# Performance work log

Hardware: AMD Instinct MI355X
Metric: run time of the kernel (lower is better)

Reference implementation:

```python
import jax, jax.numpy as jnp
import numpy as np

WIDTH = 64
HEIGHT = 64
FEAT = 128
LAT = 64
NUM_SLOTS = 7


def pixel_coords(img_size):
    g = jnp.linspace(-1.0, 1.0, img_size)
    g1, g2 = jnp.meshgrid(g, g, indexing='ij')  # matches torch.meshgrid default
    return jnp.stack([g1, g2], axis=0)[None]  # (1, 2, S, S)


def clamp_pg(x, lo, hi):
    # clamp that preserves gradients (straight-through)
    return x + jax.lax.stop_gradient(jnp.clip(x, lo, hi) - x)


def setup_inputs() -> dict:
    key = jax.random.key(0)
    k0, k1, k2, k3 = jax.random.split(key, 4)
    bs = 64
    x = jax.random.normal(k0, (bs, FEAT, WIDTH, HEIGHT), jnp.float32)
    rand_pixel = jax.random.uniform(k1, (bs, 1, WIDTH, HEIGHT), jnp.float32)
    conv_w = jax.random.normal(k2, (LAT, FEAT), jnp.float32) / np.sqrt(FEAT)
    conv_b = jax.random.normal(k3, (LAT,), jnp.float32) * 0.01
    gate = jnp.asarray(0.5, jnp.float32)  # ScalarGate parameter (nonzero so c_f is non-degenerate)
    # laplacian kernel: sigma_init = 1 / (sqrt(num_slots) * log 2)
    log_sigma = jnp.asarray(np.log(1.0 / (np.sqrt(NUM_SLOTS) * np.log(2.0))), jnp.float32)
    return {'x': x, 'rand_pixel': rand_pixel, 'conv_w': conv_w, 'conv_b': conv_b,
            'gate': gate, 'log_sigma': log_sigma, 'num_cl_steps': 6}


def _forward(x, rand_pixel, conv_w, conv_b, gate, log_sigma, num_cl_steps):
    bs = x.shape[0]
    # SemiConv: gated 1x1 conv + fixed uv coordinate channels
    out = gate * (jnp.einsum('of,bfhw->bohw', conv_w, x) + conv_b[None, :, None, None])
    uv = jnp.concatenate([jnp.zeros((1, LAT - 2, WIDTH, HEIGHT), out.dtype),
                          pixel_coords(WIDTH).astype(out.dtype)], axis=1)
    c_f = out + uv                      # (bs, LAT, W, H)
    delta = out[:, -2:]                 # (bs, 2, W, H)
    sigma = jnp.exp(log_sigma)
    c_flat = c_f.reshape(bs, LAT, -1)   # (bs, LAT, W*H)
    b_idx = jnp.arange(bs)
    log_s0 = jnp.zeros((bs, 1, WIDTH, HEIGHT), c_f.dtype)

    def step(log_s, _):
        # interpolate-to-same-size is identity -> scope = exp(log_s)
        probs = (rand_pixel * jnp.exp(log_s)).reshape(bs, -1)
        idx = jnp.argmax(probs, axis=1)                 # (bs,)
        seed = c_flat[b_idx, :, idx]                    # (bs, LAT)
        diff = c_f - seed[:, :, None, None]
        dist = jnp.sqrt(clamp_pg((diff ** 2).sum(1), 1e-10, 1e10))  # euclidian (laplacian kernel)
        alpha = jnp.exp(-dist / sigma)[:, None]         # (bs, 1, W, H)
        alpha = clamp_pg(alpha, 0.01, 0.99)
        log_m = log_s + jnp.log(alpha)
        new_log_s = log_s + jnp.log1p(-alpha)
        return new_log_s, (log_m, new_log_s, seed)

    log_s_final, (log_m_steps, log_s_steps, seeds) = jax.lax.scan(
        step, log_s0, None, length=num_cl_steps)
    # log_m_k has num_cl_steps masks plus the final scope appended
    log_m_k = jnp.concatenate([log_m_steps, log_s_final[None]], axis=0)
    log_s_k = jnp.concatenate([log_s0[None], log_s_steps], axis=0)
    return log_m_k, log_s_k, c_f, delta, seeds


def reference(x, rand_pixel, conv_w, conv_b, gate, log_sigma, num_cl_steps):
    return _forward(x, rand_pixel, conv_w, conv_b, gate, log_sigma, num_cl_steps)
```

## Files before the change

kernel.cpp:

```cpp
#include <hip/hip_runtime.h>
#include <hip/hip_bf16.h>

#define NPIX 4096
#define FEAT 128
#define LAT 64
#define BS 64
#define NSTEPS 6

#define OFF_LOGM  0u
#define OFF_LOGS  1835008u
#define OFF_CF    3670016u
#define OFF_DELTA 20447232u
#define OFF_SEEDS 20971520u

typedef float f32x4 __attribute__((ext_vector_type(4)));
typedef short s16x8 __attribute__((ext_vector_type(8)));

__device__ __forceinline__ void amax_comb(float& bv, int& bi, float v, int i) {
    if (v > bv || (v == bv && i < bi)) { bv = v; bi = i; }
}

__device__ __forceinline__ short f2bf_rne(float r) {
    __hip_bfloat16 h = __float2bfloat16(r);
    return __builtin_bit_cast(short, h);
}

__device__ __forceinline__ void split2(float v, short& hi, short& lo) {
    unsigned u = __builtin_bit_cast(unsigned, v);
    hi = (short)(u >> 16);
    float hf = __builtin_bit_cast(float, u & 0xFFFF0000u);
    lo = f2bf_rne(v - hf);
}

__device__ __forceinline__ void transpose4(float4& v, int b) {
    float4 w;
    w.x = __shfl_xor(v.x, 1, 64); w.y = __shfl_xor(v.y, 1, 64);
    w.z = __shfl_xor(v.z, 1, 64); w.w = __shfl_xor(v.w, 1, 64);
    float4 u;
    if ((b & 1) == 0) u = make_float4(v.x, w.x, v.z, w.z);
    else              u = make_float4(w.y, v.y, w.w, v.w);
    float4 w2;
    w2.x = __shfl_xor(u.x, 2, 64); w2.y = __shfl_xor(u.y, 2, 64);
    w2.z = __shfl_xor(u.z, 2, 64); w2.w = __shfl_xor(u.w, 2, 64);
    if ((b & 2) == 0) v = make_float4(u.x, u.y, w2.x, w2.y);
    else              v = make_float4(w2.z, w2.w, u.z, u.w);
}

__global__ void prep_w(const float* __restrict__ w, const float* __restrict__ gate_p,
                       short* __restrict__ gwh, short* __restrict__ gwl)
{
    int i = blockIdx.x * 256 + threadIdx.x;
    float v = gate_p[0] * w[i];
    short h, l; split2(v, h, l);
    gwh[i] = h; gwl[i] = l;
}

__global__ __launch_bounds__(512, 4) void conv_mfma(
    const float* __restrict__ x, const float* __restrict__ rand_pixel,
    const float* __restrict__ bias, const float* __restrict__ gate_p,
    float* __restrict__ out,
    float* __restrict__ pval, int* __restrict__ pidx, int* __restrict__ cnt,
    const short* __restrict__ gwh, const short* __restrict__ gwl)
{
    __shared__ __align__(16) short Xhi[256][40];
    __shared__ __align__(16) short Xlo[256][40];
    __shared__ __align__(16) short Whi[64][132];
    __shared__ __align__(16) short Wlo[64][132];
    __shared__ float sbias[64];

    const int tid  = threadIdx.x;
    const int b    = blockIdx.x >> 4;
    const int tile = blockIdx.x & 15;
    const int p0   = tile * 256;
    const int lane = tid & 63;
    const int wv   = tid >> 6;
    const int l15  = lane & 15;
    const int lg   = lane >> 4;
    const int oh   = wv >> 2;
    const int pxq  = wv & 3;

    const int q  = tid >> 2;
    const int j  = tid & 3;
    const int P  = (q & 63) * 4;
    const int g0 = q >> 6;

    if (tile == 0 && tid < 8) cnt[b * 8 + tid] = 0;
    if (tid < 64) sbias[tid] = gate_p[0] * bias[tid];

    {
        const int o = tid >> 3, c = (tid & 7) * 16;
        *(s16x8*)&Whi[o][c]     = *(const s16x8*)&gwh[o * 128 + c];
        *(s16x8*)&Whi[o][c + 8] = *(const s16x8*)&gwh[o * 128 + c + 8];
        *(s16x8*)&Wlo[o][c]     = *(const s16x8*)&gwl[o * 128 + c];
        *(s16x8*)&Wlo[o][c + 8] = *(const s16x8*)&gwl[o * 128 + c + 8];
    }

    const float* xb = x + (size_t)b * FEAT * NPIX + p0;
    float4 v[4];
    #pragma unroll
    for (int i = 0; i < 4; ++i) {
        int g = g0 + 2 * i;
        v[i] = *(const float4*)(xb + (size_t)(g * 4 + j) * NPIX + P);
    }
    #pragma unroll
    for (int i = 0; i < 4; ++i) {
        int g = g0 + 2 * i;
        float4 t = v[i]; transpose4(t, j);
        short h0, l0, h1, l1, h2, l2, h3, l3;
        split2(t.x, h0, l0); split2(t.y, h1, l1);
        split2(t.z, h2, l2); split2(t.w, h3, l3);
        *(short4*)&Xhi[P + j][g * 4] = make_short4(h0, h1, h2, h3);
        *(short4*)&Xlo[P + j][g * 4] = make_short4(l0, l1, l2, l3);
    }
    __syncthreads();

    f32x4 acc[2][4];
    #pragma unroll
    for (int og2 = 0; og2 < 2; ++og2)
        #pragma unroll
        for (int pg = 0; pg < 4; ++pg)
            acc[og2][pg] = (f32x4){0.f, 0.f, 0.f, 0.f};

    #pragma unroll
    for (int kc = 0; kc < 4; ++kc) {
        if (kc < 3) {
            #pragma unroll
            for (int i = 0; i < 4; ++i) {
                int g = g0 + 2 * i;
                v[i] = *(const float4*)(xb + (size_t)((kc + 1) * 32 + g * 4 + j) * NPIX + P);
            }
        }

        s16x8 Ah[2], Al[2];
        #pragma unroll
        for (int og2 = 0; og2 < 2; ++og2) {
            int o = oh * 32 + og2 * 16 + l15;
            Ah[og2] = *(const s16x8*)&Whi[o][kc * 32 + lg * 8];
            Al[og2] = *(const s16x8*)&Wlo[o][kc * 32 + lg * 8];
        }

        #pragma unroll
        for (int pg = 0; pg < 4; ++pg) {
            int pxl = pxq * 64 + pg * 16 + l15;
            s16x8 Bh = *(const s16x8*)&Xhi[pxl][lg * 8];
            s16x8 Bl = *(const s16x8*)&Xlo[pxl][lg * 8];
            #pragma unroll
            for (int og2 = 0; og2 < 2; ++og2) {
                acc[og2][pg] = __builtin_amdgcn_mfma_f32_16x16x32_bf16(Ah[og2], Bh, acc[og2][pg], 0, 0, 0);
                acc[og2][pg] = __builtin_amdgcn_mfma_f32_16x16x32_bf16(Ah[og2], Bl, acc[og2][pg], 0, 0, 0);
                acc[og2][pg] = __builtin_amdgcn_mfma_f32_16x16x32_bf16(Al[og2], Bh, acc[og2][pg], 0, 0, 0);
            }
        }

        if (kc < 3) {
            __syncthreads();
            #pragma unroll
            for (int i = 0; i < 4; ++i) {
                int g = g0 + 2 * i;
                float4 t = v[i]; transpose4(t, j);
                short h0, l0, h1, l1, h2, l2, h3, l3;
                split2(t.x, h0, l0); split2(t.y, h1, l1);
                split2(t.z, h2, l2); split2(t.w, h3, l3);
                *(short4*)&Xhi[P + j][g * 4] = make_short4(h0, h1, h2, h3);
                *(short4*)&Xlo[P + j][g * 4] = make_short4(l0, l1, l2, l3);
            }
            __syncthreads();
        }
    }

    float* cf = out + OFF_CF + (size_t)b * LAT * NPIX;
    #pragma unroll
    for (int og2 = 0; og2 < 2; ++og2) {
        #pragma unroll
        for (int pg = 0; pg < 4; ++pg) {
            #pragma unroll
            for (int r = 0; r < 4; ++r) {
                int o = oh * 32 + og2 * 16 + lg * 4 + r;
                int p = p0 + pxq * 64 + pg * 16 + l15;
                float vv = acc[og2][pg][r] + sbias[o];
                if (o == 62) {
                    out[OFF_DELTA + ((size_t)b * 2 + 0) * NPIX + p] = vv;
                    vv += (float)(-1.0 + 2.0 * (double)(p >> 6) / 63.0);
                } else if (o == 63) {
                    out[OFF_DELTA + ((size_t)b * 2 + 1) * NPIX + p] = vv;
                    vv += (float)(-1.0 + 2.0 * (double)(p & 63) / 63.0);
                }
                cf[(size_t)o * NPIX + p] = vv;
            }
        }
    }

    if (wv == 0) {
        *(float4*)(out + OFF_LOGS + (size_t)b * NPIX + p0 + lane * 4) =
            make_float4(0.f, 0.f, 0.f, 0.f);
        float4 rv = *(const float4*)(rand_pixel + (size_t)b * NPIX + p0 + lane * 4);
        int pb = p0 + lane * 4;
        float bv = rv.x; int bi = pb;
        if (rv.y > bv) { bv = rv.y; bi = pb + 1; }
        if (rv.z > bv) { bv = rv.z; bi = pb + 2; }
        if (rv.w > bv) { bv = rv.w; bi = pb + 3; }
        #pragma unroll
        for (int off = 32; off > 0; off >>= 1) {
            float ov = __shfl_down(bv, off, 64);
            int   oi = __shfl_down(bi, off, 64);
            amax_comb(bv, bi, ov, oi);
        }
        if (lane == 0) { pval[blockIdx.x] = bv; pidx[blockIdx.x] = bi; }
    }
}

#define REP16(OP) OP(0) OP(1) OP(2) OP(3) OP(4) OP(5) OP(6) OP(7) \
                  OP(8) OP(9) OP(10) OP(11) OP(12) OP(13) OP(14) OP(15)

__global__ __launch_bounds__(1024) void steps_fused(
    const float* __restrict__ rand_pixel, const float* __restrict__ log_sigma_p,
    float* __restrict__ out, float* pv, int* pi, int* cnt)
{
    __shared__ float s_mv[16];
    __shared__ int   s_mi[16];
    __shared__ __align__(16) float s_seed[LAT];
    __shared__ float s_rv[16];
    __shared__ int   s_ri[16];

    const int tid  = threadIdx.x;
    const int b    = blockIdx.x >> 2;
    const int tile = blockIdx.x & 3;
    const int p    = tile * 1024 + tid;

    const float* cfb = out + OFF_CF + (size_t)b * LAT * NPIX;

#define DECLR(i) f32x4 r##i;
    REP16(DECLR)
#define LOADR(i) r##i = (f32x4){ cfb[(size_t)(4*i+0)*NPIX + p], cfb[(size_t)(4*i+1)*NPIX + p], \
                                 cfb[(size_t)(4*i+2)*NPIX + p], cfb[(size_t)(4*i+3)*NPIX + p] };
    REP16(LOADR)

    f32x4 aq = r0 * r0;
#define SQR(i) aq += r##i * r##i;
    SQR(1) SQR(2) SQR(3) SQR(4) SQR(5) SQR(6) SQR(7)
    SQR(8) SQR(9) SQR(10) SQR(11) SQR(12) SQR(13) SQR(14) SQR(15)
    const float cr2 = aq[0] + aq[1] + aq[2] + aq[3];

    const float rp    = rand_pixel[(size_t)b * NPIX + p];
    const float sigma = expf(log_sigma_p[0]);
    float ls = 0.f;

    #pragma unroll 1
    for (int s = 0; s < NSTEPS; ++s) {
        if (s > 0) {
            if (tid == 0) {
                while (__hip_atomic_load(&cnt[b * 8 + s], __ATOMIC_ACQUIRE,
                                         __HIP_MEMORY_SCOPE_AGENT) < 4)
                    __builtin_amdgcn_s_sleep(2);
            }
            __syncthreads();
        }
        const int nmerge = (s == 0) ? 16 : 4;
        if (tid < nmerge) {
            s_mv[tid] = __hip_atomic_load(&pv[(s * BS + b) * 16 + tid],
                                          __ATOMIC_RELAXED, __HIP_MEMORY_SCOPE_AGENT);
            s_mi[tid] = __hip_atomic_load(&pi[(s * BS + b) * 16 + tid],
                                          __ATOMIC_RELAXED, __HIP_MEMORY_SCOPE_AGENT);
        }
        __syncthreads();

        float bv = -1.0f; int bi = 0;
        for (int k = 0; k < nmerge; ++k) amax_comb(bv, bi, s_mv[k], s_mi[k]);

        if (tid < LAT) s_seed[tid] = cfb[(size_t)tid * NPIX + bi];
        __syncthreads();
        if (tile == 0 && tid < LAT)
            out[OFF_SEEDS + ((size_t)s * BS + b) * LAT + tid] = s_seed[tid];

        f32x4 dacc = (f32x4){0.f, 0.f, 0.f, 0.f};
        f32x4 sacc = (f32x4){0.f, 0.f, 0.f, 0.f};
#define DOT(i) { f32x4 sv = *(const f32x4*)&s_seed[4*i]; dacc += r##i * sv; sacc += sv * sv; }
        REP16(DOT)
        float dot = dacc[0] + dacc[1] + dacc[2] + dacc[3];
        float s2  = sacc[0] + sacc[1] + sacc[2] + sacc[3];
        float d2  = cr2 + s2 - 2.0f * dot;

        float dist  = sqrtf(fminf(fmaxf(d2, 1e-10f), 1e10f));
        float alpha = expf(-dist / sigma);
        alpha = fminf(fmaxf(alpha, 0.01f), 0.99f);
        float lm  = ls + logf(alpha);
        float lsn = ls + log1pf(-alpha);

        out[OFF_LOGM + ((size_t)s * BS + b) * NPIX + p]       = lm;
        out[OFF_LOGS + ((size_t)(s + 1) * BS + b) * NPIX + p] = lsn;
        ls = lsn;

        if (s == NSTEPS - 1) {
            out[OFF_LOGM + ((size_t)NSTEPS * BS + b) * NPIX + p] = lsn;
        } else {
            float prob = rp * expf(lsn);
            int   idx  = p;
            #pragma unroll
            for (int off = 32; off > 0; off >>= 1) {
                float ov = __shfl_down(prob, off, 64);
                int   oi = __shfl_down(idx, off, 64);
                amax_comb(prob, idx, ov, oi);
            }
            int lane = tid & 63, wid = tid >> 6;
            if (lane == 0) { s_rv[wid] = prob; s_ri[wid] = idx; }
            __syncthreads();
            if (tid == 0) {
                float fb = s_rv[0]; int fi = s_ri[0];
                #pragma unroll
                for (int k = 1; k < 16; ++k) amax_comb(fb, fi, s_rv[k], s_ri[k]);
                __hip_atomic_store(&pv[((s + 1) * BS + b) * 16 + tile], fb,
                                   __ATOMIC_RELAXED, __HIP_MEMORY_SCOPE_AGENT);
                __hip_atomic_store(&pi[((s + 1) * BS + b) * 16 + tile], fi,
                                   __ATOMIC_RELAXED, __HIP_MEMORY_SCOPE_AGENT);
                __hip_atomic_fetch_add(&cnt[b * 8 + s + 1], 1,
                                       __ATOMIC_RELEASE, __HIP_MEMORY_SCOPE_AGENT);
            }
        }
    }
}

__global__ __launch_bounds__(1024) void step_kernel(
    const float* __restrict__ rand_pixel, const float* __restrict__ log_sigma_p,
    float* __restrict__ out, float* pv, int* pi, int step)
{
    __shared__ float s_mv[16];
    __shared__ int   s_mi[16];
    __shared__ __align__(16) float s_seed[LAT];
    __shared__ float s_rv[16];
    __shared__ int   s_ri[16];

    const int tid  = threadIdx.x;
    const int b    = blockIdx.x >> 2;
    const int tile = blockIdx.x & 3;
    const int p    = tile * 1024 + tid;

    const float* cfb = out + OFF_CF + (size_t)b * LAT * NPIX;

    const int nmerge = (step == 0) ? 16 : 4;
    if (tid < nmerge) { s_mv[tid] = pv[(step * BS + b) * 16 + tid];
                        s_mi[tid] = pi[(step * BS + b) * 16 + tid]; }
    __syncthreads();
    float bv = -1.0f; int bi = 0;
    for (int k = 0; k < nmerge; ++k) amax_comb(bv, bi, s_mv[k], s_mi[k]);

    if (tid < LAT) s_seed[tid] = cfb[(size_t)tid * NPIX + bi];
    __syncthreads();
    if (tile == 0 && tid < LAT)
        out[OFF_SEEDS + ((size_t)step * BS + b) * LAT + tid] = s_seed[tid];

    float d2 = 0.f;
    #pragma unroll
    for (int c = 0; c < LAT; ++c) {
        float d = cfb[(size_t)c * NPIX + p] - s_seed[c];
        d2 = fmaf(d, d, d2);
    }
    float dist  = sqrtf(fminf(fmaxf(d2, 1e-10f), 1e10f));
    float sigma = expf(log_sigma_p[0]);
    float alpha = expf(-dist / sigma);
    alpha = fminf(fmaxf(alpha, 0.01f), 0.99f);

    float ls  = out[OFF_LOGS + ((size_t)step * BS + b) * NPIX + p];
    float lm  = ls + logf(alpha);
    float lsn = ls + log1pf(-alpha);

    out[OFF_LOGM + ((size_t)step * BS + b) * NPIX + p]       = lm;
    out[OFF_LOGS + ((size_t)(step + 1) * BS + b) * NPIX + p] = lsn;
    if (step == NSTEPS - 1)
        out[OFF_LOGM + ((size_t)NSTEPS * BS + b) * NPIX + p] = lsn;

    if (step < NSTEPS - 1) {
        float prob = rand_pixel[(size_t)b * NPIX + p] * expf(lsn);
        int   idx  = p;
        #pragma unroll
        for (int off = 32; off > 0; off >>= 1) {
            float ov = __shfl_down(prob, off, 64);
            int   oi = __shfl_down(idx, off, 64);
            amax_comb(prob, idx, ov, oi);
        }
        int lane = tid & 63, wid = tid >> 6;
        if (lane == 0) { s_rv[wid] = prob; s_ri[wid] = idx; }
        __syncthreads();
        if (tid == 0) {
            float fb = s_rv[0]; int fi = s_ri[0];
            #pragma unroll
            for (int k = 1; k < 16; ++k) amax_comb(fb, fi, s_rv[k], s_ri[k]);
            pv[((step + 1) * BS + b) * 16 + tile] = fb;
            pi[((step + 1) * BS + b) * 16 + tile] = fi;
        }
    }
}

extern "C" void kernel_launch(void* const* d_in, const int* in_sizes, int n_in,
                              void* d_out, int out_size, void* d_ws, size_t ws_size,
                              hipStream_t stream) {
    const float* x          = (const float*)d_in[0];
    const float* rand_pixel = (const float*)d_in[1];
    const float* w          = (const float*)d_in[2];
    const float* bias       = (const float*)d_in[3];
    const float* gate       = (const float*)d_in[4];
    const float* log_sigma  = (const float*)d_in[5];

    float* out = (float*)d_out;
    float* pv  = (float*)d_ws;
    int*   pi  = (int*)((char*)d_ws + 24576);
    int*   cnt = (int*)((char*)d_ws + 49152);
    short* gwh = (short*)((char*)d_ws + 51200);
    short* gwl = (short*)((char*)d_ws + 67584);

    prep_w<<<32, 256, 0, stream>>>(w, gate, gwh, gwl);
    conv_mfma<<<1024, 512, 0, stream>>>(x, rand_pixel, bias, gate, out,
                                        pv, pi, cnt, gwh, gwl);

    const float* a0 = rand_pixel; const float* a1 = log_sigma; float* a2 = out;
    float* a3 = pv; int* a4 = pi; int* a5 = cnt;
    void* kp[6] = {(void*)&a0, (void*)&a1, (void*)&a2, (void*)&a3, (void*)&a4, (void*)&a5};
    hipError_t e = hipLaunchCooperativeKernel((const void*)steps_fused,
                                              dim3(256), dim3(1024), kp, 0, stream);
    if (e != hipSuccess) {
        for (int s = 0; s < NSTEPS; ++s)
            step_kernel<<<256, 1024, 0, stream>>>(rand_pixel, log_sigma, out, pv, pi, s);
    }
}
```

Measured before the change: 131.7 us.

## Split step kernel into 16 tiles of 256 threads per batch and compute direct diffs

The persistent step kernel now runs 1024 blocks of 256 threads, 16 tiles per batch image, instead of 256 blocks of 1024 threads. The per-step merge reads 16 partial argmax entries, and each block waits for 16 arrivals instead of 4. The distance is now computed as a sum of squared differences rather than norm expansion, dropping the precomputed squared norm. This trades more inter-block sync traffic and more seed gathers for smaller blocks that may schedule better. The direct differences are also more accurate.

```diff
diff --git a/kernel.cpp b/kernel.cpp
--- a/kernel.cpp
+++ b/kernel.cpp
@@ -212,20 +212,20 @@
 #define REP16(OP) OP(0) OP(1) OP(2) OP(3) OP(4) OP(5) OP(6) OP(7) \
                   OP(8) OP(9) OP(10) OP(11) OP(12) OP(13) OP(14) OP(15)
 
-__global__ __launch_bounds__(1024) void steps_fused(
+__global__ __launch_bounds__(256, 4) void steps_fused(
     const float* __restrict__ rand_pixel, const float* __restrict__ log_sigma_p,
     float* __restrict__ out, float* pv, int* pi, int* cnt)
 {
     __shared__ float s_mv[16];
     __shared__ int   s_mi[16];
     __shared__ __align__(16) float s_seed[LAT];
-    __shared__ float s_rv[16];
-    __shared__ int   s_ri[16];
+    __shared__ float s_rv[4];
+    __shared__ int   s_ri[4];
 
     const int tid  = threadIdx.x;
-    const int b    = blockIdx.x >> 2;
-    const int tile = blockIdx.x & 3;
-    const int p    = tile * 1024 + tid;
+    const int b    = blockIdx.x >> 4;
+    const int tile = blockIdx.x & 15;
+    const int p    = tile * 256 + tid;
 
     const float* cfb = out + OFF_CF + (size_t)b * LAT * NPIX;
 
@@ -235,12 +235,6 @@
                                  cfb[(size_t)(4*i+2)*NPIX + p], cfb[(size_t)(4*i+3)*NPIX + p] };
     REP16(LOADR)
 
-    f32x4 aq = r0 * r0;
-#define SQR(i) aq += r##i * r##i;
-    SQR(1) SQR(2) SQR(3) SQR(4) SQR(5) SQR(6) SQR(7)
-    SQR(8) SQR(9) SQR(10) SQR(11) SQR(12) SQR(13) SQR(14) SQR(15)
-    const float cr2 = aq[0] + aq[1] + aq[2] + aq[3];
-
     const float rp    = rand_pixel[(size_t)b * NPIX + p];
     const float sigma = expf(log_sigma_p[0]);
     float ls = 0.f;
@@ -250,13 +244,12 @@
         if (s > 0) {
             if (tid == 0) {
                 while (__hip_atomic_load(&cnt[b * 8 + s], __ATOMIC_ACQUIRE,
-                                         __HIP_MEMORY_SCOPE_AGENT) < 4)
+                                         __HIP_MEMORY_SCOPE_AGENT) < 16)
                     __builtin_amdgcn_s_sleep(2);
             }
             __syncthreads();
         }
-        const int nmerge = (s == 0) ? 16 : 4;
-        if (tid < nmerge) {
+        if (tid < 16) {
             s_mv[tid] = __hip_atomic_load(&pv[(s * BS + b) * 16 + tid],
                                           __ATOMIC_RELAXED, __HIP_MEMORY_SCOPE_AGENT);
             s_mi[tid] = __hip_atomic_load(&pi[(s * BS + b) * 16 + tid],
@@ -265,7 +258,8 @@
         __syncthreads();
 
         float bv = -1.0f; int bi = 0;
-        for (int k = 0; k < nmerge; ++k) amax_comb(bv, bi, s_mv[k], s_mi[k]);
+        #pragma unroll
+        for (int k = 0; k < 16; ++k) amax_comb(bv, bi, s_mv[k], s_mi[k]);
 
         if (tid < LAT) s_seed[tid] = cfb[(size_t)tid * NPIX + bi];
         __syncthreads();
@@ -273,12 +267,9 @@
             out[OFF_SEEDS + ((size_t)s * BS + b) * LAT + tid] = s_seed[tid];
 
         f32x4 dacc = (f32x4){0.f, 0.f, 0.f, 0.f};
-        f32x4 sacc = (f32x4){0.f, 0.f, 0.f, 0.f};
-#define DOT(i) { f32x4 sv = *(const f32x4*)&s_seed[4*i]; dacc += r##i * sv; sacc += sv * sv; }
-        REP16(DOT)
-        float dot = dacc[0] + dacc[1] + dacc[2] + dacc[3];
-        float s2  = sacc[0] + sacc[1] + sacc[2] + sacc[3];
-        float d2  = cr2 + s2 - 2.0f * dot;
+#define DIFF(i) { f32x4 sv = *(const f32x4*)&s_seed[4*i]; f32x4 dv = r##i - sv; dacc += dv * dv; }
+        REP16(DIFF)
+        float d2 = dacc[0] + dacc[1] + dacc[2] + dacc[3];
 
         float dist  = sqrtf(fminf(fmaxf(d2, 1e-10f), 1e10f));
         float alpha = expf(-dist / sigma);
@@ -307,7 +298,7 @@
             if (tid == 0) {
                 float fb = s_rv[0]; int fi = s_ri[0];
                 #pragma unroll
-                for (int k = 1; k < 16; ++k) amax_comb(fb, fi, s_rv[k], s_ri[k]);
+                for (int k = 1; k < 4; ++k) amax_comb(fb, fi, s_rv[k], s_ri[k]);
                 __hip_atomic_store(&pv[((s + 1) * BS + b) * 16 + tile], fb,
                                    __ATOMIC_RELAXED, __HIP_MEMORY_SCOPE_AGENT);
                 __hip_atomic_store(&pi[((s + 1) * BS + b) * 16 + tile], fi,
@@ -319,29 +310,29 @@
     }
 }
 
-__global__ __launch_bounds__(1024) void step_kernel(
+__global__ __launch_bounds__(256, 4) void step_kernel(
     const float* __restrict__ rand_pixel, const float* __restrict__ log_sigma_p,
     float* __restrict__ out, float* pv, int* pi, int step)
 {
     __shared__ float s_mv[16];
     __shared__ int   s_mi[16];
     __shared__ __align__(16) float s_seed[LAT];
-    __shared__ float s_rv[16];
-    __shared__ int   s_ri[16];
+    __shared__ float s_rv[4];
+    __shared__ int   s_ri[4];
 
     const int tid  = threadIdx.x;
-    const int b    = blockIdx.x >> 2;
-    const int tile = blockIdx.x & 3;
-    const int p    = tile * 1024 + tid;
+    const int b    = blockIdx.x >> 4;
+    const int tile = blockIdx.x & 15;
+    const int p    = tile * 256 + tid;
 
     const float* cfb = out + OFF_CF + (size_t)b * LAT * NPIX;
 
-    const int nmerge = (step == 0) ? 16 : 4;
-    if (tid < nmerge) { s_mv[tid] = pv[(step * BS + b) * 16 + tid];
-                        s_mi[tid] = pi[(step * BS + b) * 16 + tid]; }
+    if (tid < 16) { s_mv[tid] = pv[(step * BS + b) * 16 + tid];
+                    s_mi[tid] = pi[(step * BS + b) * 16 + tid]; }
     __syncthreads();
     float bv = -1.0f; int bi = 0;
-    for (int k = 0; k < nmerge; ++k) amax_comb(bv, bi, s_mv[k], s_mi[k]);
+    #pragma unroll
+    for (int k = 0; k < 16; ++k) amax_comb(bv, bi, s_mv[k], s_mi[k]);
 
     if (tid < LAT) s_seed[tid] = cfb[(size_t)tid * NPIX + bi];
     __syncthreads();
@@ -383,7 +374,7 @@
         if (tid == 0) {
             float fb = s_rv[0]; int fi = s_ri[0];
             #pragma unroll
-            for (int k = 1; k < 16; ++k) amax_comb(fb, fi, s_rv[k], s_ri[k]);
+            for (int k = 1; k < 4; ++k) amax_comb(fb, fi, s_rv[k], s_ri[k]);
             pv[((step + 1) * BS + b) * 16 + tile] = fb;
             pi[((step + 1) * BS + b) * 16 + tile] = fi;
         }
@@ -415,9 +406,9 @@
     float* a3 = pv; int* a4 = pi; int* a5 = cnt;
     void* kp[6] = {(void*)&a0, (void*)&a1, (void*)&a2, (void*)&a3, (void*)&a4, (void*)&a5};
     hipError_t e = hipLaunchCooperativeKernel((const void*)steps_fused,
-                                              dim3(256), dim3(1024), kp, 0, stream);
+                                              dim3(1024), dim3(256), kp, 0, stream);
     if (e != hipSuccess) {
         for (int s = 0; s < NSTEPS; ++s)
-            step_kernel<<<256, 1024, 0, stream>>>(rand_pixel, log_sigma, out, pv, pi, s);
-    }
-}
+            step_kernel<<<1024, 256, 0, stream>>>(rand_pixel, log_sigma, out, pv, pi, s);
+    }
+}
```

New measurement: 252.3 us. 91.6% more time.

## Park c_f rows in AGPRs, use direct diff-square, and remap block-to-batch order

Applied to the files above, without the earlier changes.

Moves the 64 per-pixel c_f values held across all steps from VGPRs into accumulation registers through inline v_accvgpr writes and reads. The distance is now computed directly as a sum of squared differences instead of the norm-expansion form. It also sets a min-blocks hint in launch_bounds and changes the blockIdx mapping so the four tiles of one batch are spread 64 blocks apart. The aim is to cut VGPR pressure so more waves stay resident. The costs are extra read instructions per step, a serial FMA chain, and a changed co-scheduling pattern that could affect the inter-block spin-wait dependencies.

```diff
diff --git a/kernel.cpp b/kernel.cpp
--- a/kernel.cpp
+++ b/kernel.cpp
@@ -212,7 +212,7 @@
 #define REP16(OP) OP(0) OP(1) OP(2) OP(3) OP(4) OP(5) OP(6) OP(7) \
                   OP(8) OP(9) OP(10) OP(11) OP(12) OP(13) OP(14) OP(15)
 
-__global__ __launch_bounds__(1024) void steps_fused(
+__global__ __launch_bounds__(1024, 4) void steps_fused(
     const float* __restrict__ rand_pixel, const float* __restrict__ log_sigma_p,
     float* __restrict__ out, float* pv, int* pi, int* cnt)
 {
@@ -223,23 +223,24 @@
     __shared__ int   s_ri[16];
 
     const int tid  = threadIdx.x;
-    const int b    = blockIdx.x >> 2;
-    const int tile = blockIdx.x & 3;
+    const int b    = blockIdx.x & 63;
+    const int tile = blockIdx.x >> 6;
     const int p    = tile * 1024 + tid;
 
     const float* cfb = out + OFF_CF + (size_t)b * LAT * NPIX;
 
-#define DECLR(i) f32x4 r##i;
-    REP16(DECLR)
-#define LOADR(i) r##i = (f32x4){ cfb[(size_t)(4*i+0)*NPIX + p], cfb[(size_t)(4*i+1)*NPIX + p], \
-                                 cfb[(size_t)(4*i+2)*NPIX + p], cfb[(size_t)(4*i+3)*NPIX + p] };
-    REP16(LOADR)
-
-    f32x4 aq = r0 * r0;
-#define SQR(i) aq += r##i * r##i;
-    SQR(1) SQR(2) SQR(3) SQR(4) SQR(5) SQR(6) SQR(7)
-    SQR(8) SQR(9) SQR(10) SQR(11) SQR(12) SQR(13) SQR(14) SQR(15)
-    const float cr2 = aq[0] + aq[1] + aq[2] + aq[3];
+#define AG_DECL(i) float ag##i##_0, ag##i##_1, ag##i##_2, ag##i##_3;
+    REP16(AG_DECL)
+#define AG_PARK(i) { \
+    float v0 = cfb[(size_t)(4*i+0)*NPIX + p]; \
+    float v1 = cfb[(size_t)(4*i+1)*NPIX + p]; \
+    float v2 = cfb[(size_t)(4*i+2)*NPIX + p]; \
+    float v3 = cfb[(size_t)(4*i+3)*NPIX + p]; \
+    asm volatile("v_accvgpr_write_b32 %0, %1" : "=a"(ag##i##_0) : "v"(v0)); \
+    asm volatile("v_accvgpr_write_b32 %0, %1" : "=a"(ag##i##_1) : "v"(v1)); \
+    asm volatile("v_accvgpr_write_b32 %0, %1" : "=a"(ag##i##_2) : "v"(v2)); \
+    asm volatile("v_accvgpr_write_b32 %0, %1" : "=a"(ag##i##_3) : "v"(v3)); }
+    REP16(AG_PARK)
 
     const float rp    = rand_pixel[(size_t)b * NPIX + p];
     const float sigma = expf(log_sigma_p[0]);
@@ -272,13 +273,18 @@
         if (tile == 0 && tid < LAT)
             out[OFF_SEEDS + ((size_t)s * BS + b) * LAT + tid] = s_seed[tid];
 
-        f32x4 dacc = (f32x4){0.f, 0.f, 0.f, 0.f};
-        f32x4 sacc = (f32x4){0.f, 0.f, 0.f, 0.f};
-#define DOT(i) { f32x4 sv = *(const f32x4*)&s_seed[4*i]; dacc += r##i * sv; sacc += sv * sv; }
-        REP16(DOT)
-        float dot = dacc[0] + dacc[1] + dacc[2] + dacc[3];
-        float s2  = sacc[0] + sacc[1] + sacc[2] + sacc[3];
-        float d2  = cr2 + s2 - 2.0f * dot;
+        float d2 = 0.f;
+#define AG_DIFF(i) { \
+        float c0, c1, c2, c3; \
+        asm volatile("v_accvgpr_read_b32 %0, %1" : "=v"(c0) : "a"(ag##i##_0)); \
+        asm volatile("v_accvgpr_read_b32 %0, %1" : "=v"(c1) : "a"(ag##i##_1)); \
+        asm volatile("v_accvgpr_read_b32 %0, %1" : "=v"(c2) : "a"(ag##i##_2)); \
+        asm volatile("v_accvgpr_read_b32 %0, %1" : "=v"(c3) : "a"(ag##i##_3)); \
+        float e0 = c0 - s_seed[4*i+0]; d2 = fmaf(e0, e0, d2); \
+        float e1 = c1 - s_seed[4*i+1]; d2 = fmaf(e1, e1, d2); \
+        float e2 = c2 - s_seed[4*i+2]; d2 = fmaf(e2, e2, d2); \
+        float e3 = c3 - s_seed[4*i+3]; d2 = fmaf(e3, e3, d2); }
+        REP16(AG_DIFF)
 
         float dist  = sqrtf(fminf(fmaxf(d2, 1e-10f), 1e10f));
         float alpha = expf(-dist / sigma);
@@ -319,7 +325,7 @@
     }
 }
 
-__global__ __launch_bounds__(1024) void step_kernel(
+__global__ __launch_bounds__(1024, 4) void step_kernel(
     const float* __restrict__ rand_pixel, const float* __restrict__ log_sigma_p,
     float* __restrict__ out, float* pv, int* pi, int step)
 {
@@ -330,8 +336,8 @@
     __shared__ int   s_ri[16];
 
     const int tid  = threadIdx.x;
-    const int b    = blockIdx.x >> 2;
-    const int tile = blockIdx.x & 3;
+    const int b    = blockIdx.x & 63;
+    const int tile = blockIdx.x >> 6;
     const int p    = tile * 1024 + tid;
 
     const float* cfb = out + OFF_CF + (size_t)b * LAT * NPIX;
```

After: 124.7 us (median of 3 runs). 1.06x faster.
